# Kernel tuning notes

Measured on AMD Instinct MI355X. Metric: run time of the kernel, lower is better.

The kernel has to match this reference:

```python
import jax, jax.numpy as jnp
import numpy as np

D_MODEL = 256; D_STATE = 64; D_CONV = 4; EXPAND = 2; HEADDIM = 64; CHUNK = 64
D_INNER = EXPAND * D_MODEL          # 512
NHEADS = D_INNER // HEADDIM         # 8
D_IN_PROJ = 2 * D_INNER + 2 * D_STATE + NHEADS   # 1160
CONV_DIM = D_INNER + 2 * D_STATE    # 640
OBS_DIM = 3; T = 4096; BK = 32; K = 4


def setup_inputs() -> dict:
    key = jax.random.key(0)
    ks = jax.random.split(key, 8)
    f = jnp.float32
    return {
        "obs": jax.random.normal(ks[0], (T, BK, OBS_DIM), f),
        "W_in": jax.random.normal(ks[1], (D_MODEL, OBS_DIM), f) * 0.1,
        "b_in": jnp.zeros((D_MODEL,), f),
        "in_proj_w": jax.random.normal(ks[2], (D_IN_PROJ, D_MODEL), f) * 0.02,
        "conv_w": jax.random.normal(ks[3], (CONV_DIM, D_CONV), f) * 0.2,
        "conv_b": jnp.zeros((CONV_DIM,), f),
        "dt_bias": jax.random.normal(ks[4], (NHEADS,), f) * 0.1,
        "A_log": jnp.log(jnp.arange(1, NHEADS + 1, dtype=f)),
        "D_param": jnp.ones((NHEADS,), f),
        "norm_w": jnp.ones((D_INNER,), f),
        "out_proj_w": jax.random.normal(ks[5], (D_MODEL, D_INNER), f) * 0.02,
        "head": jnp.zeros((1,), f),
        "log_tau": jnp.zeros((1,), f),
        "k": K,
    }


def segsum(x):
    """Stable segment-sum: x (..., T) -> (..., T, T) lower-triangular cumulative sums."""
    L = x.shape[-1]
    x = jnp.broadcast_to(x[..., None], (*x.shape, L))
    x = jnp.where(jnp.tril(jnp.ones((L, L), bool), -1), x, 0.0)
    s = jnp.cumsum(x, axis=-2)
    return jnp.where(jnp.tril(jnp.ones((L, L), bool), 0), s, -jnp.inf)


def ssd(x, A, B, C, chunk):
    """Mamba2 SSD. x:(b,l,h,p) A:(b,l,h) B,C:(b,l,n). Returns y:(b,l,h,p), final state."""
    b, l, h, p = x.shape
    c = l // chunk
    x = x.reshape(b, c, chunk, h, p)
    A = A.reshape(b, c, chunk, h).transpose(0, 3, 1, 2)        # (b,h,c,l)
    B = B.reshape(b, c, chunk, -1)
    C = C.reshape(b, c, chunk, -1)
    A_cs = jnp.cumsum(A, axis=-1)                              # (b,h,c,l)
    Lmat = jnp.exp(segsum(A))                                  # (b,h,c,l,s)
    Y_diag = jnp.einsum('bcln,bcsn,bhcls,bcshp->bclhp', C, B, Lmat, x)
    decay_states = jnp.exp(A_cs[..., -1:] - A_cs)              # (b,h,c,l)
    states = jnp.einsum('bcln,bhcl,bclhp->bchpn', B, decay_states, x)
    states = jnp.concatenate([jnp.zeros_like(states[:, :1]), states], axis=1)
    decay_chunk = jnp.exp(segsum(jnp.pad(A_cs[..., -1], ((0, 0), (0, 0), (1, 0)))))
    new_states = jnp.einsum('bhzc,bchpn->bzhpn', decay_chunk, states)
    states, final = new_states[:, :-1], new_states[:, -1]
    Y_off = jnp.einsum('bcln,bchpn,bhcl->bclhp', C, states, jnp.exp(A_cs))
    return (Y_diag + Y_off).reshape(b, l, h, p), final


def reference(obs, W_in, b_in, in_proj_w, conv_w, conv_b, dt_bias, A_log, D_param,
              norm_w, out_proj_w, head, log_tau, k):
    Tt, Bk, _ = obs.shape
    x = obs @ W_in.T + b_in                        # (T,Bk,d_model)  input linear
    u = jnp.transpose(x, (1, 0, 2))                # (Bk,T,d_model)
    zxbcdt = u @ in_proj_w.T                       # (Bk,T,d_in_proj)
    z = zxbcdt[..., :D_INNER]
    xBC = zxbcdt[..., D_INNER:D_INNER + CONV_DIM]
    dt = jax.nn.softplus(zxbcdt[..., D_INNER + CONV_DIM:] + dt_bias)   # (B,T,h)
    # causal depthwise conv1d + silu (kernel D_CONV)
    xp = jnp.pad(xBC, ((0, 0), (D_CONV - 1, 0), (0, 0)))
    conv = conv_b
    for i in range(D_CONV):
        conv = conv + xp[:, i:i + Tt, :] * conv_w[:, i]
    xBC = jax.nn.silu(conv)
    xs = xBC[..., :D_INNER].reshape(Bk, Tt, NHEADS, HEADDIM)
    Bm = xBC[..., D_INNER:D_INNER + D_STATE]
    Cm = xBC[..., D_INNER + D_STATE:]
    A = -jnp.exp(A_log)                            # (h,)
    y, _final = ssd(xs * dt[..., None], A * dt, Bm, Cm, CHUNK)
    y = y + xs * D_param[None, None, :, None]
    y = y.reshape(Bk, Tt, D_INNER)
    # gated RMSNorm
    y = y * jax.nn.silu(z)
    y = y * jax.lax.rsqrt(jnp.mean(y * y, axis=-1, keepdims=True) + 1e-5) * norm_w
    y = y @ out_proj_w.T                           # (Bk,T,d_model)
    y = jnp.transpose(y, (1, 0, 2))                # (T,Bk,d_model)
    q = jnp.sum(y, axis=-1) * jax.nn.softplus(head)  # (T,Bk)
    q = q.reshape(Tt, -1, k)
    logits = q / jnp.exp(log_tau)
    return (q, logits)
```

## Files before the change

kernel.cpp:

```cpp
#include <hip/hip_runtime.h>

#define TLEN 4096
#define NBK  32

typedef __attribute__((ext_vector_type(8))) short short8;
typedef __attribute__((ext_vector_type(8))) unsigned short ushort8;
typedef __attribute__((ext_vector_type(4))) unsigned short ushort4v;
typedef __attribute__((ext_vector_type(4))) float f32x4;

#define OFF_WC 0
#define OFF_BC 3480
#define OFF_W3 4640
#define OFF_TB 12320
#define OFF_NW 14880
#define OFF_Y_BYTES 262144

__device__ __forceinline__ unsigned short f2bf(float f){
  unsigned int u = __float_as_uint(f);
  u = (u + 0x7FFFu + ((u >> 16) & 1u)) >> 16;
  return (unsigned short)u;
}
__device__ __forceinline__ float bf2f(unsigned short h){
  return __uint_as_float(((unsigned int)h) << 16);
}
__device__ __forceinline__ float softplusf_(float x){
  return (x > 15.f) ? x : log1pf(__expf(x));
}
__device__ __forceinline__ float siluf_(float x){
  return x * __fdividef(1.f, 1.f + __expf(-x));
}

__global__ void prep1_kernel(const float* __restrict__ ipw,
                             const float* __restrict__ W_in,
                             const float* __restrict__ b_in,
                             float* __restrict__ wsf){
  int r = blockIdx.x*256 + threadIdx.x;
  if (r >= 1160) return;
  const float* row = ipw + (size_t)r*256;
  float a0=0.f,a1=0.f,a2=0.f,ab=0.f;
  for (int m=0;m<256;m++){
    float w = row[m];
    a0 = fmaf(w, W_in[m*3+0], a0);
    a1 = fmaf(w, W_in[m*3+1], a1);
    a2 = fmaf(w, W_in[m*3+2], a2);
    ab = fmaf(w, b_in[m], ab);
  }
  wsf[OFF_WC + r*3+0]=a0; wsf[OFF_WC + r*3+1]=a1; wsf[OFF_WC + r*3+2]=a2;
  wsf[OFF_BC + r]=ab;
}

__global__ void prep2_kernel(const float* __restrict__ conv_w,
                             const float* __restrict__ norm_w,
                             const float* __restrict__ out_proj_w,
                             float* __restrict__ wsf){
  int r = blockIdx.x*256 + threadIdx.x;
  if (r < 640){
    float bc = wsf[OFF_BC + 512 + r];
    #pragma unroll
    for (int i=0;i<4;i++){
      float cw = conv_w[r*4+i];
      wsf[OFF_TB + r*4+i] = cw*bc;
      wsf[OFF_W3 + r*12 + i*3+0] = cw * wsf[OFF_WC + (512+r)*3+0];
      wsf[OFF_W3 + r*12 + i*3+1] = cw * wsf[OFF_WC + (512+r)*3+1];
      wsf[OFF_W3 + r*12 + i*3+2] = cw * wsf[OFF_WC + (512+r)*3+2];
    }
  }
  if (r < 512){
    float s=0.f;
    for (int m=0;m<256;m++) s += out_proj_w[(size_t)m*512 + r];
    wsf[OFF_NW + r] = norm_w[r]*s;
  }
}

#define SW(row_, col_) ((row_)*64 + ((col_) ^ (((row_)&7)<<3)))

__global__ __launch_bounds__(1024, 1) void ssd_kernel(
    const float* __restrict__ obs, const float* __restrict__ conv_b,
    const float* __restrict__ dt_bias, const float* __restrict__ A_log,
    const float* __restrict__ D_param, const float* __restrict__ wsf,
    unsigned short* __restrict__ Yg)
{
  __shared__ __align__(16) unsigned short obs_b[3*4096];
  __shared__ __align__(16) unsigned short W3T[192*40];
  __shared__ __align__(16) unsigned short OW[2][64*40];
  __shared__ float dt_l[4096];
  __shared__ float acs_l[4096];
  __shared__ float CBe[192];
  __shared__ float TBl[192*4];
  __shared__ __align__(16) unsigned short Bs[64*64], BDTl[64*64], Cs[64*64],
      CEl[64*64], XDT[64*64], XSl[64*64], Mm[64*64], Sb[64*64];

  const int tid  = threadIdx.x;
  const int b    = blockIdx.x >> 3;
  const int h    = blockIdx.x & 7;
  const int lane = tid & 63;
  const int wid  = tid >> 6;
  const int tm   = wid >> 2, tn = wid & 3;

  const int am    = tm*16 + (lane & 15);
  const int bn    = tn*16 + (lane & 15);
  const int rbase = tm*16 + ((lane>>4)&3)*4;

  for (int idx = tid; idx < 3*4096; idx += 1024){
    int j = idx >> 12, t = idx & 4095;
    obs_b[idx] = f2bf(obs[(size_t)t*(NBK*3) + b*3 + j]);
  }
  for (int idx = tid; idx < 192*28; idx += 1024){
    int row = idx/28; W3T[row*40 + 12 + (idx - row*28)] = 0;
  }
  for (int idx = tid; idx < 2*64*28; idx += 1024){
    int row = idx/28; (&OW[0][0])[row*40 + 12 + (idx - row*28)] = 0;
  }
  for (int idx = tid; idx < 192*12; idx += 1024){
    int lc = idx/12, ij = idx - lc*12;
    int ch = (lc<64) ? h*64+lc : 448+lc;
    W3T[lc*40 + ij] = f2bf(wsf[OFF_W3 + ch*12 + ij]);
  }
  for (int idx = tid; idx < 192; idx += 1024){
    int ch = (idx<64) ? h*64+idx : 448+idx;
    float s = conv_b[ch];
    #pragma unroll
    for (int i=0;i<4;i++){ float tb = wsf[OFF_TB + ch*4 + i]; TBl[idx*4+i] = tb; s += tb; }
    CBe[idx] = s;
  }
  const float Wd0 = wsf[OFF_WC+(1152+h)*3+0], Wd1 = wsf[OFF_WC+(1152+h)*3+1],
              Wd2 = wsf[OFF_WC+(1152+h)*3+2];
  const float bdt = wsf[OFF_BC + 1152 + h] + dt_bias[h];
  const float A_h = -__expf(A_log[h]);
  const float Dh  = D_param[h];
  for (int cc = wid; cc < 64; cc += 16){
    int t = cc*64 + lane;
    const float* ob = obs + (size_t)t*(NBK*3) + b*3;
    float draw = bdt + Wd0*ob[0] + Wd1*ob[1] + Wd2*ob[2];
    float dtv = softplusf_(draw);
    float a = A_h * dtv;
    #pragma unroll
    for (int o=1;o<64;o<<=1){
      float u = __shfl_up(a, o);
      if (lane >= o) a += u;
    }
    dt_l[t] = dtv; acs_l[t] = a;
  }
  __syncthreads();

  short8 afrag[3];
  #pragma unroll
  for (int e=0;e<3;e++){
    int idx = wid*3+e, ct = idx>>2;
    afrag[e] = *(const short8*)&W3T[(ct*16 + (lane&15))*40 + ((lane>>4)&3)*8];
  }
  if (tid < 768){
    int tt_ = tid/12, ij = tid - tt_*12;
    int i = ij/3, j = ij - i*3;
    int ts = tt_ - 3 + i;
    OW[0][tt_*40 + ij] = (ts >= 0) ? obs_b[j*4096 + ts] : (unsigned short)0;
  }
  __syncthreads();

  f32x4 sreg = {0.f,0.f,0.f,0.f};

  for (int c = 0; c < 64; ++c){
    const int t0 = c*64;
    const float At = acs_l[t0 + 63];

    {
      ushort4v sp;
      #pragma unroll
      for (int r=0;r<4;r++) sp[r] = f2bf(sreg[r]);
      *(ushort4v*)&Sb[SW(bn, rbase)] = sp;

      f32x4 g[3];
      #pragma unroll
      for (int e=0;e<3;e++){
        int idx = wid*3+e, tt = idx&3;
        const short8 bf = *(const short8*)&OW[c&1][(tt*16 + (lane&15))*40 + ((lane>>4)&3)*8];
        f32x4 z0 = {0.f,0.f,0.f,0.f};
        g[e] = __builtin_amdgcn_mfma_f32_16x16x32_bf16(afrag[e], bf, z0, 0, 0, 0);
      }
      #pragma unroll
      for (int e=0;e<3;e++){
        const int idx = wid*3+e, ct = idx>>2, tt = idx&3;
        const int t_  = tt*16 + (lane&15);
        const int chb = ct*16 + ((lane>>4)&3)*4;
        float dtt  = dt_l[t0 + t_];
        float acst = acs_l[t0 + t_];
        float dcy  = __expf(At - acst);
        float eAc  = __expf(acst);
        float v[4];
        #pragma unroll
        for (int r=0;r<4;r++){
          float pre = g[e][r] + CBe[chb+r];
          if (c==0 && tt==0){
            int tq = lane&15;
            if (tq < 3){
              #pragma unroll
              for (int i2=0;i2<3;i2++) if (i2 < 3-tq) pre -= TBl[(chb+r)*4+i2];
            }
          }
          v[r] = siluf_(pre);
        }
        if (ct < 4){
          int cb = chb;
          ushort4v xs_;
          #pragma unroll
          for (int r=0;r<4;r++) xs_[r] = f2bf(v[r]);
          *(ushort4v*)&XSl[SW(t_, cb)] = xs_;
          #pragma unroll
          for (int r=0;r<4;r++) XDT[SW(cb+r, t_)] = f2bf(v[r]*dtt);
        } else if (ct < 8){
          int nb = chb - 64;
          ushort4v b_;
          #pragma unroll
          for (int r=0;r<4;r++) b_[r] = f2bf(v[r]);
          *(ushort4v*)&Bs[SW(t_, nb)] = b_;
          #pragma unroll
          for (int r=0;r<4;r++) BDTl[SW(nb+r, t_)] = f2bf(v[r]*dcy);
        } else {
          int nb = chb - 128;
          ushort4v c_, ce_;
          #pragma unroll
          for (int r=0;r<4;r++){ c_[r] = f2bf(v[r]); ce_[r] = f2bf(v[r]*eAc); }
          *(ushort4v*)&Cs[SW(t_, nb)]  = c_;
          *(ushort4v*)&CEl[SW(t_, nb)] = ce_;
        }
      }
      if (c < 63 && tid < 768){
        int tt_ = tid/12, ij = tid - tt_*12;
        int i = ij/3, j = ij - i*3;
        int ts = (c+1)*64 + tt_ - 3 + i;
        OW[(c+1)&1][tt_*40 + ij] = obs_b[j*4096 + ts];
      }
    }
    __syncthreads();

    {
      f32x4 g2 = {0.f,0.f,0.f,0.f};
      #pragma unroll
      for (int k=0;k<2;k++){
        int kb = k*32 + ((lane>>4)&3)*8;
        const short8 av = *(const short8*)&Cs[SW(am, kb)];
        const short8 bv = *(const short8*)&Bs[SW(bn, kb)];
        g2 = __builtin_amdgcn_mfma_f32_16x16x32_bf16(av, bv, g2, 0, 0, 0);
      }
      float acS = acs_l[t0 + bn];
      #pragma unroll
      for (int r=0;r<4;r++){
        int lrow = rbase + r;
        float acl = acs_l[t0 + lrow];
        float mv = (lrow >= bn) ? g2[r]*__expf(acl - acS) : 0.f;
        Mm[SW(lrow, bn)] = f2bf(mv);
      }
    }
    __syncthreads();

    {
      f32x4 y = {0.f,0.f,0.f,0.f};
      #pragma unroll
      for (int k=0;k<2;k++){
        int kb = k*32 + ((lane>>4)&3)*8;
        const short8 av = *(const short8*)&Mm[SW(am, kb)];
        const short8 bv = *(const short8*)&XDT[SW(bn, kb)];
        y = __builtin_amdgcn_mfma_f32_16x16x32_bf16(av, bv, y, 0, 0, 0);
      }
      #pragma unroll
      for (int k=0;k<2;k++){
        int kb = k*32 + ((lane>>4)&3)*8;
        const short8 av = *(const short8*)&CEl[SW(am, kb)];
        const short8 bv = *(const short8*)&Sb[SW(bn, kb)];
        y = __builtin_amdgcn_mfma_f32_16x16x32_bf16(av, bv, y, 0, 0, 0);
      }
      float eAtot = __expf(At);
      #pragma unroll
      for (int r=0;r<4;r++) sreg[r] *= eAtot;
      #pragma unroll
      for (int k=0;k<2;k++){
        int kb = k*32 + ((lane>>4)&3)*8;
        const short8 av = *(const short8*)&BDTl[SW(am, kb)];
        const short8 bv = *(const short8*)&XDT[SW(bn, kb)];
        sreg = __builtin_amdgcn_mfma_f32_16x16x32_bf16(av, bv, sreg, 0, 0, 0);
      }
      #pragma unroll
      for (int r=0;r<4;r++){
        int lrow = rbase + r;
        float xsv = bf2f(XSl[SW(lrow, bn)]);
        Yg[((size_t)(b*4096 + t0 + lrow))*512 + h*64 + bn] = f2bf(y[r] + xsv*Dh);
      }
    }
    __syncthreads();
  }
}

__global__ __launch_bounds__(256) void final_kernel(
    const unsigned short* __restrict__ Yg, const float* __restrict__ obs,
    const float* __restrict__ wsf, const float* __restrict__ head,
    const float* __restrict__ log_tau, float* __restrict__ out)
{
  __shared__ float Wz[512*3];
  __shared__ float bz[512];
  __shared__ float nwl[512];
  int tid = threadIdx.x;
  for (int i=tid; i<512*3; i+=256) Wz[i] = wsf[OFF_WC + i];
  for (int i=tid; i<512; i+=256){ bz[i] = wsf[OFF_BC+i]; nwl[i] = wsf[OFF_NW+i]; }
  __syncthreads();
  int wid = tid>>6, lane = tid&63;
  float hsc  = softplusf_(head[0]);
  float itau = __expf(-log_tau[0]);
  int base = blockIdx.x*64 + wid*16;
  for (int rr=0; rr<16; ++rr){
    int row = base + rr;
    int bb = row >> 12, t = row & 4095;
    const float* ob = obs + (size_t)t*(NBK*3) + bb*3;
    float o0=ob[0], o1=ob[1], o2=ob[2];
    ushort8 yv = *(const ushort8*)&Yg[(size_t)row*512 + lane*8];
    float s2=0.f, sq=0.f;
    #pragma unroll
    for (int u=0;u<8;u++){
      int i = lane*8+u;
      float yf = bf2f(yv[u]);
      float z = bz[i] + Wz[i*3]*o0 + Wz[i*3+1]*o1 + Wz[i*3+2]*o2;
      float yg = yf * siluf_(z);
      s2 = fmaf(yg, yg, s2);
      sq = fmaf(yg, nwl[i], sq);
    }
    #pragma unroll
    for (int o=32;o;o>>=1){ s2 += __shfl_xor(s2,o); sq += __shfl_xor(sq,o); }
    if (lane==0){
      float rms = rsqrtf(s2*(1.f/512.f) + 1e-5f);
      float q = sq * rms * hsc;
      out[(size_t)t*32 + bb] = q;
      out[131072 + (size_t)t*32 + bb] = q * itau;
    }
  }
}

extern "C" void kernel_launch(void* const* d_in, const int* in_sizes, int n_in,
                              void* d_out, int out_size, void* d_ws, size_t ws_size,
                              hipStream_t stream) {
  (void)in_sizes; (void)n_in; (void)out_size; (void)ws_size;
  const float* obs        = (const float*)d_in[0];
  const float* W_in       = (const float*)d_in[1];
  const float* b_in       = (const float*)d_in[2];
  const float* in_proj_w  = (const float*)d_in[3];
  const float* conv_w     = (const float*)d_in[4];
  const float* conv_b     = (const float*)d_in[5];
  const float* dt_bias    = (const float*)d_in[6];
  const float* A_log      = (const float*)d_in[7];
  const float* D_param    = (const float*)d_in[8];
  const float* norm_w     = (const float*)d_in[9];
  const float* out_proj_w = (const float*)d_in[10];
  const float* head       = (const float*)d_in[11];
  const float* log_tau    = (const float*)d_in[12];
  float* wsf = (float*)d_ws;
  unsigned short* Yg = (unsigned short*)((char*)d_ws + OFF_Y_BYTES);
  float* out = (float*)d_out;

  prep1_kernel<<<5, 256, 0, stream>>>(in_proj_w, W_in, b_in, wsf);
  prep2_kernel<<<3, 256, 0, stream>>>(conv_w, norm_w, out_proj_w, wsf);
  ssd_kernel<<<256, 1024, 0, stream>>>(obs, conv_b, dt_bias, A_log, D_param, wsf, Yg);
  final_kernel<<<2048, 256, 0, stream>>>(Yg, obs, wsf, head, log_tau, out);
}
```

Baseline: 456.7 us.

## Double-buffer SSD chunk staging, fold D skip into diagonal, parallelize prep reductions

The SSD kernel now double-buffers the per-chunk B/C/X tiles. The conv projection for chunk c+1 (and the obs window for c+2) is computed while chunk c's matmuls run, so one barrier per chunk goes away. The D skip term is folded into the diagonal of the intra-chunk mask matrix, which removes the XS buffer. Decay exponentials are precomputed once, packed bf16 conversion instructions are used, and the obs staging buffer is dropped. prep1 switches to one wave per row with shuffle reductions, and final_kernel keeps its weights in registers and uses strided Yg loads. More shared memory is used, and folding D/dt into a bf16 matrix may cost precision.

```diff
diff --git a/kernel.cpp b/kernel.cpp
--- a/kernel.cpp
+++ b/kernel.cpp
@@ -1,12 +1,8 @@
 #include <hip/hip_runtime.h>
 
-#define TLEN 4096
-#define NBK  32
-
 typedef __attribute__((ext_vector_type(8))) short short8;
-typedef __attribute__((ext_vector_type(8))) unsigned short ushort8;
-typedef __attribute__((ext_vector_type(4))) unsigned short ushort4v;
 typedef __attribute__((ext_vector_type(4))) float f32x4;
+typedef __attribute__((ext_vector_type(2))) unsigned int uint2v;
 
 #define OFF_WC 0
 #define OFF_BC 3480
@@ -23,30 +19,46 @@
 __device__ __forceinline__ float bf2f(unsigned short h){
   return __uint_as_float(((unsigned int)h) << 16);
 }
+__device__ __forceinline__ unsigned int cvtpk(float lo, float hi){
+  unsigned int r;
+  asm("v_cvt_pk_bf16_f32 %0, %1, %2" : "=v"(r) : "v"(lo), "v"(hi));
+  return r;
+}
 __device__ __forceinline__ float softplusf_(float x){
   return (x > 15.f) ? x : log1pf(__expf(x));
 }
 __device__ __forceinline__ float siluf_(float x){
   return x * __fdividef(1.f, 1.f + __expf(-x));
 }
+
+#define SW(row_, col_) ((row_)*64 + ((col_) ^ (((row_)&7)<<3)))
 
 __global__ void prep1_kernel(const float* __restrict__ ipw,
                              const float* __restrict__ W_in,
                              const float* __restrict__ b_in,
                              float* __restrict__ wsf){
-  int r = blockIdx.x*256 + threadIdx.x;
-  if (r >= 1160) return;
-  const float* row = ipw + (size_t)r*256;
+  int gw = (blockIdx.x*256 + threadIdx.x) >> 6;
+  int lane = threadIdx.x & 63;
+  if (gw >= 1160) return;
+  const float* row = ipw + (size_t)gw*256;
   float a0=0.f,a1=0.f,a2=0.f,ab=0.f;
-  for (int m=0;m<256;m++){
+  #pragma unroll
+  for (int m = lane; m < 256; m += 64){
     float w = row[m];
     a0 = fmaf(w, W_in[m*3+0], a0);
     a1 = fmaf(w, W_in[m*3+1], a1);
     a2 = fmaf(w, W_in[m*3+2], a2);
     ab = fmaf(w, b_in[m], ab);
   }
-  wsf[OFF_WC + r*3+0]=a0; wsf[OFF_WC + r*3+1]=a1; wsf[OFF_WC + r*3+2]=a2;
-  wsf[OFF_BC + r]=ab;
+  #pragma unroll
+  for (int o=32;o;o>>=1){
+    a0 += __shfl_xor(a0,o); a1 += __shfl_xor(a1,o);
+    a2 += __shfl_xor(a2,o); ab += __shfl_xor(ab,o);
+  }
+  if (lane==0){
+    wsf[OFF_WC + gw*3+0]=a0; wsf[OFF_WC + gw*3+1]=a1; wsf[OFF_WC + gw*3+2]=a2;
+    wsf[OFF_BC + gw]=ab;
+  }
 }
 
 __global__ void prep2_kernel(const float* __restrict__ conv_w,
@@ -72,56 +84,60 @@
   }
 }
 
-#define SW(row_, col_) ((row_)*64 + ((col_) ^ (((row_)&7)<<3)))
-
-__global__ __launch_bounds__(1024, 1) void ssd_kernel(
+__global__ __launch_bounds__(1024, 4) void ssd_kernel(
     const float* __restrict__ obs, const float* __restrict__ conv_b,
     const float* __restrict__ dt_bias, const float* __restrict__ A_log,
     const float* __restrict__ D_param, const float* __restrict__ wsf,
     unsigned short* __restrict__ Yg)
 {
-  __shared__ __align__(16) unsigned short obs_b[3*4096];
-  __shared__ __align__(16) unsigned short W3T[192*40];
+  __shared__ __align__(16) float acs_l[4096];
+  __shared__ __align__(16) float dt_l[4096];
+  __shared__ __align__(16) unsigned short eAc_l[4096];
+  __shared__ __align__(16) unsigned short dcy_l[4096];
+  __shared__ __align__(16) unsigned short BsT[2*4096];
+  __shared__ __align__(16) unsigned short CsT[2*4096];
+  __shared__ __align__(16) unsigned short CET[2*4096];
+  __shared__ __align__(16) unsigned short XDTt[2*4096];
+  __shared__ __align__(16) unsigned short BDTt[2*4096];
+  __shared__ __align__(16) unsigned short MmSb[2*4096];
   __shared__ __align__(16) unsigned short OW[2][64*40];
-  __shared__ float dt_l[4096];
-  __shared__ float acs_l[4096];
   __shared__ float CBe[192];
-  __shared__ float TBl[192*4];
-  __shared__ __align__(16) unsigned short Bs[64*64], BDTl[64*64], Cs[64*64],
-      CEl[64*64], XDT[64*64], XSl[64*64], Mm[64*64], Sb[64*64];
 
   const int tid  = threadIdx.x;
   const int b    = blockIdx.x >> 3;
   const int h    = blockIdx.x & 7;
   const int lane = tid & 63;
   const int wid  = tid >> 6;
+  const int ln15 = lane & 15;
+  const int quad = (lane >> 4) & 3;
+  const int quad4 = quad*4, quad8 = quad*8;
   const int tm   = wid >> 2, tn = wid & 3;
-
-  const int am    = tm*16 + (lane & 15);
-  const int bn    = tn*16 + (lane & 15);
-  const int rbase = tm*16 + ((lane>>4)&3)*4;
-
-  for (int idx = tid; idx < 3*4096; idx += 1024){
-    int j = idx >> 12, t = idx & 4095;
-    obs_b[idx] = f2bf(obs[(size_t)t*(NBK*3) + b*3 + j]);
-  }
-  for (int idx = tid; idx < 192*28; idx += 1024){
-    int row = idx/28; W3T[row*40 + 12 + (idx - row*28)] = 0;
-  }
-  for (int idx = tid; idx < 2*64*28; idx += 1024){
-    int row = idx/28; (&OW[0][0])[row*40 + 12 + (idx - row*28)] = 0;
-  }
-  for (int idx = tid; idx < 192*12; idx += 1024){
-    int lc = idx/12, ij = idx - lc*12;
-    int ch = (lc<64) ? h*64+lc : 448+lc;
-    W3T[lc*40 + ij] = f2bf(wsf[OFF_W3 + ch*12 + ij]);
-  }
-  for (int idx = tid; idx < 192; idx += 1024){
-    int ch = (idx<64) ? h*64+idx : 448+idx;
+  const int am    = tm*16 + ln15;
+  const int bn    = tn*16 + ln15;
+  const int rbase = tm*16 + quad4;
+
+  unsigned short* const Mm  = MmSb;
+  unsigned short* const Sb  = MmSb + 4096;
+  unsigned short* const W3T = MmSb;
+
+  for (int i = tid; i < 192*40; i += 1024){
+    int lc = i/40, k = i - lc*40;
+    unsigned short v = 0;
+    if (k < 12){
+      int ch = (lc<64) ? h*64+lc : 448+lc;
+      v = f2bf(wsf[OFF_W3 + ch*12 + k]);
+    }
+    W3T[i] = v;
+  }
+  for (int i = tid; i < 2*64*28; i += 1024){
+    int r = i/28; (&OW[0][0])[r*40 + 12 + (i - r*28)] = 0;
+  }
+  if (tid < 192){
+    int ch = (tid<64) ? h*64+tid : 448+tid;
     float s = conv_b[ch];
     #pragma unroll
-    for (int i=0;i<4;i++){ float tb = wsf[OFF_TB + ch*4 + i]; TBl[idx*4+i] = tb; s += tb; }
-    CBe[idx] = s;
+    for (int i=0;i<4;i++) s += wsf[OFF_TB + ch*4 + i];
+    CBe[tid] = s;
   }
   const float Wd0 = wsf[OFF_WC+(1152+h)*3+0], Wd1 = wsf[OFF_WC+(1152+h)*3+1],
               Wd2 = wsf[OFF_WC+(1152+h)*3+2];
@@ -130,7 +146,7 @@
   const float Dh  = D_param[h];
   for (int cc = wid; cc < 64; cc += 16){
     int t = cc*64 + lane;
-    const float* ob = obs + (size_t)t*(NBK*3) + b*3;
+    const float* ob = obs + (size_t)t*96 + b*3;
     float draw = bdt + Wd0*ob[0] + Wd1*ob[1] + Wd2*ob[2];
     float dtv = softplusf_(draw);
     float a = A_h * dtv;
@@ -139,151 +155,182 @@
       float u = __shfl_up(a, o);
       if (lane >= o) a += u;
     }
-    dt_l[t] = dtv; acs_l[t] = a;
+    float At = __shfl(a, 63);
+    dt_l[t]  = dtv;
+    acs_l[t] = a;
+    eAc_l[t] = f2bf(__expf(a));
+    dcy_l[t] = f2bf(__expf(At - a));
   }
   __syncthreads();
 
-  short8 afrag[3];
+  short8 afrag1[2], afrag2[2];
+  float  cbe1[2][4], cbe2[2];
   #pragma unroll
-  for (int e=0;e<3;e++){
-    int idx = wid*3+e, ct = idx>>2;
-    afrag[e] = *(const short8*)&W3T[(ct*16 + (lane&15))*40 + ((lane>>4)&3)*8];
-  }
-  if (tid < 768){
-    int tt_ = tid/12, ij = tid - tt_*12;
-    int i = ij/3, j = ij - i*3;
-    int ts = tt_ - 3 + i;
-    OW[0][tt_*40 + ij] = (ts >= 0) ? obs_b[j*4096 + ts] : (unsigned short)0;
-  }
+  for (int e=0;e<2;e++){
+    const int idx = wid*2+e;
+    const int ct1 = 4 + (idx & 7);
+    afrag1[e] = *(const short8*)&W3T[(ct1*16 + ln15)*40 + quad8];
+    #pragma unroll
+    for (int r=0;r<4;r++) cbe1[e][r] = CBe[ct1*16 + quad4 + r];
+    const int ct2 = idx & 7;
+    afrag2[e] = *(const short8*)&W3T[(ct2*16 + ln15)*40 + quad8];
+    cbe2[e] = CBe[ct2*16 + ln15];
+  }
+
+  auto PREFOW = [&](int cn){
+    if (tid < 768){
+      int tt_ = tid/12, ij = tid - tt_*12;
+      int i = ij/3, j = ij - i*3;
+      int ts = cn*64 + tt_ - 3 + i;
+      OW[cn&1][tt_*40 + ij] = (ts >= 0) ? f2bf(obs[(size_t)ts*96 + b*3 + j])
+                                        : (unsigned short)0;
+    }
+  };
+  PREFOW(0);
+  PREFOW(1);
   __syncthreads();
 
-  f32x4 sreg = {0.f,0.f,0.f,0.f};
-
-  for (int c = 0; c < 64; ++c){
-    const int t0 = c*64;
-    const float At = acs_l[t0 + 63];
-
-    {
-      ushort4v sp;
-      #pragma unroll
-      for (int r=0;r<4;r++) sp[r] = f2bf(sreg[r]);
-      *(ushort4v*)&Sb[SW(bn, rbase)] = sp;
-
-      f32x4 g[3];
-      #pragma unroll
-      for (int e=0;e<3;e++){
-        int idx = wid*3+e, tt = idx&3;
-        const short8 bf = *(const short8*)&OW[c&1][(tt*16 + (lane&15))*40 + ((lane>>4)&3)*8];
+  auto STAGE = [&](int cn, int pn){
+    unsigned short* Bp  = BsT  + pn*4096;
+    unsigned short* Cp  = CsT  + pn*4096;
+    unsigned short* CEp = CET  + pn*4096;
+    unsigned short* Xp  = XDTt + pn*4096;
+    unsigned short* BDp = BDTt + pn*4096;
+    const int tW0 = cn*64;
+    #pragma unroll
+    for (int e=0;e<2;e++){
+      const int idx = wid*2+e;
+      const int tt  = idx >> 3;
+      const short8 owf = *(const short8*)&OW[cn&1][(tt*16 + ln15)*40 + quad8];
+      {
+        const int ct1 = 4 + (idx & 7);
+        const int chb = ct1*16 + quad4;
+        const int t_  = tt*16 + ln15;
         f32x4 z0 = {0.f,0.f,0.f,0.f};
-        g[e] = __builtin_amdgcn_mfma_f32_16x16x32_bf16(afrag[e], bf, z0, 0, 0, 0);
-      }
-      #pragma unroll
-      for (int e=0;e<3;e++){
-        const int idx = wid*3+e, ct = idx>>2, tt = idx&3;
-        const int t_  = tt*16 + (lane&15);
-        const int chb = ct*16 + ((lane>>4)&3)*4;
-        float dtt  = dt_l[t0 + t_];
-        float acst = acs_l[t0 + t_];
-        float dcy  = __expf(At - acst);
-        float eAc  = __expf(acst);
+        f32x4 g = __builtin_amdgcn_mfma_f32_16x16x32_bf16(afrag1[e], owf, z0, 0,0,0);
         float v[4];
         #pragma unroll
         for (int r=0;r<4;r++){
-          float pre = g[e][r] + CBe[chb+r];
-          if (c==0 && tt==0){
-            int tq = lane&15;
-            if (tq < 3){
-              #pragma unroll
-              for (int i2=0;i2<3;i2++) if (i2 < 3-tq) pre -= TBl[(chb+r)*4+i2];
-            }
+          float pre = g[r] + cbe1[e][r];
+          if (cn==0 && tt==0 && ln15 < 3){
+            int chg = 448 + chb + r;
+            #pragma unroll
+            for (int i2=0;i2<3;i2++) if (i2 < 3-ln15) pre -= wsf[OFF_TB + chg*4 + i2];
           }
           v[r] = siluf_(pre);
         }
-        if (ct < 4){
-          int cb = chb;
-          ushort4v xs_;
-          #pragma unroll
-          for (int r=0;r<4;r++) xs_[r] = f2bf(v[r]);
-          *(ushort4v*)&XSl[SW(t_, cb)] = xs_;
-          #pragma unroll
-          for (int r=0;r<4;r++) XDT[SW(cb+r, t_)] = f2bf(v[r]*dtt);
-        } else if (ct < 8){
+        if (ct1 < 8){
           int nb = chb - 64;
-          ushort4v b_;
-          #pragma unroll
-          for (int r=0;r<4;r++) b_[r] = f2bf(v[r]);
-          *(ushort4v*)&Bs[SW(t_, nb)] = b_;
-          #pragma unroll
-          for (int r=0;r<4;r++) BDTl[SW(nb+r, t_)] = f2bf(v[r]*dcy);
+          *(uint2v*)&Bp[SW(t_, nb)] = (uint2v){cvtpk(v[0],v[1]), cvtpk(v[2],v[3])};
         } else {
           int nb = chb - 128;
-          ushort4v c_, ce_;
-          #pragma unroll
-          for (int r=0;r<4;r++){ c_[r] = f2bf(v[r]); ce_[r] = f2bf(v[r]*eAc); }
-          *(ushort4v*)&Cs[SW(t_, nb)]  = c_;
-          *(ushort4v*)&CEl[SW(t_, nb)] = ce_;
+          *(uint2v*)&Cp[SW(t_, nb)] = (uint2v){cvtpk(v[0],v[1]), cvtpk(v[2],v[3])};
+          float ea = bf2f(eAc_l[tW0 + t_]);
+          *(uint2v*)&CEp[SW(t_, nb)] =
+            (uint2v){cvtpk(v[0]*ea, v[1]*ea), cvtpk(v[2]*ea, v[3]*ea)};
         }
       }
-      if (c < 63 && tid < 768){
-        int tt_ = tid/12, ij = tid - tt_*12;
-        int i = ij/3, j = ij - i*3;
-        int ts = (c+1)*64 + tt_ - 3 + i;
-        OW[(c+1)&1][tt_*40 + ij] = obs_b[j*4096 + ts];
-      }
-    }
-    __syncthreads();
-
+      {
+        const int ct2 = idx & 7;
+        const int ch2 = ct2*16 + ln15;
+        const int tb2 = tt*16 + quad4;
+        f32x4 z0 = {0.f,0.f,0.f,0.f};
+        f32x4 g = __builtin_amdgcn_mfma_f32_16x16x32_bf16(owf, afrag2[e], z0, 0,0,0);
+        float v[4];
+        #pragma unroll
+        for (int r=0;r<4;r++){
+          float pre = g[r] + cbe2[e];
+          if (cn==0 && tt==0 && quad==0 && r<3){
+            int chg = (ch2<64) ? h*64+ch2 : 448+ch2;
+            #pragma unroll
+            for (int i2=0;i2<3;i2++) if (i2 < 3-r) pre -= wsf[OFF_TB + chg*4 + i2];
+          }
+          v[r] = siluf_(pre);
+        }
+        if (ct2 < 4){
+          float m0 = v[0]*dt_l[tW0+tb2+0], m1 = v[1]*dt_l[tW0+tb2+1];
+          float m2 = v[2]*dt_l[tW0+tb2+2], m3 = v[3]*dt_l[tW0+tb2+3];
+          *(uint2v*)&Xp[SW(ch2, tb2)] = (uint2v){cvtpk(m0,m1), cvtpk(m2,m3)};
+        } else {
+          int nb = ch2 - 64;
+          float m0 = v[0]*bf2f(dcy_l[tW0+tb2+0]), m1 = v[1]*bf2f(dcy_l[tW0+tb2+1]);
+          float m2 = v[2]*bf2f(dcy_l[tW0+tb2+2]), m3 = v[3]*bf2f(dcy_l[tW0+tb2+3]);
+          *(uint2v*)&BDp[SW(nb, tb2)] = (uint2v){cvtpk(m0,m1), cvtpk(m2,m3)};
+        }
+      }
+    }
+  };
+
+  STAGE(0, 0);
+  __syncthreads();
+
+  f32x4 sreg = {0.f,0.f,0.f,0.f};
+
+  for (int c = 0; c < 64; ++c){
+    const int t0 = c*64;
+    const int p  = c & 1;
+    const unsigned short* Bp  = BsT  + p*4096;
+    const unsigned short* Cp  = CsT  + p*4096;
+    const unsigned short* CEp = CET  + p*4096;
+    const unsigned short* Xp  = XDTt + p*4096;
+    const unsigned short* BDp = BDTt + p*4096;
+
+    *(uint2v*)&Sb[SW(bn, rbase)] = (uint2v){cvtpk(sreg[0],sreg[1]), cvtpk(sreg[2],sreg[3])};
+    if (c < 63) STAGE(c+1, (c+1)&1);
+    if (c < 62) PREFOW(c+2);
     {
       f32x4 g2 = {0.f,0.f,0.f,0.f};
       #pragma unroll
       for (int k=0;k<2;k++){
-        int kb = k*32 + ((lane>>4)&3)*8;
-        const short8 av = *(const short8*)&Cs[SW(am, kb)];
-        const short8 bv = *(const short8*)&Bs[SW(bn, kb)];
+        int kb = k*32 + quad8;
+        const short8 av = *(const short8*)&Bp[SW(am, kb)];
+        const short8 bv = *(const short8*)&Cp[SW(bn, kb)];
         g2 = __builtin_amdgcn_mfma_f32_16x16x32_bf16(av, bv, g2, 0, 0, 0);
       }
-      float acS = acs_l[t0 + bn];
+      float acB  = acs_l[t0 + bn];
+      float diag = __fdividef(Dh, dt_l[t0 + bn]);
+      float mv[4];
       #pragma unroll
       for (int r=0;r<4;r++){
-        int lrow = rbase + r;
-        float acl = acs_l[t0 + lrow];
-        float mv = (lrow >= bn) ? g2[r]*__expf(acl - acS) : 0.f;
-        Mm[SW(lrow, bn)] = f2bf(mv);
-      }
+        int srow = rbase + r;
+        float m_ = (bn >= srow) ? g2[r]*__expf(acB - acs_l[t0 + srow]) : 0.f;
+        if (bn == srow) m_ += diag;
+        mv[r] = m_;
+      }
+      *(uint2v*)&Mm[SW(bn, rbase)] = (uint2v){cvtpk(mv[0],mv[1]), cvtpk(mv[2],mv[3])};
     }
     __syncthreads();
 
     {
+      short8 xf[2];
+      #pragma unroll
+      for (int k=0;k<2;k++) xf[k] = *(const short8*)&Xp[SW(bn, k*32 + quad8)];
       f32x4 y = {0.f,0.f,0.f,0.f};
       #pragma unroll
       for (int k=0;k<2;k++){
-        int kb = k*32 + ((lane>>4)&3)*8;
+        int kb = k*32 + quad8;
         const short8 av = *(const short8*)&Mm[SW(am, kb)];
-        const short8 bv = *(const short8*)&XDT[SW(bn, kb)];
-        y = __builtin_amdgcn_mfma_f32_16x16x32_bf16(av, bv, y, 0, 0, 0);
+        y = __builtin_amdgcn_mfma_f32_16x16x32_bf16(av, xf[k], y, 0, 0, 0);
       }
       #pragma unroll
       for (int k=0;k<2;k++){
-        int kb = k*32 + ((lane>>4)&3)*8;
-        const short8 av = *(const short8*)&CEl[SW(am, kb)];
+        int kb = k*32 + quad8;
+        const short8 av = *(const short8*)&CEp[SW(am, kb)];
         const short8 bv = *(const short8*)&Sb[SW(bn, kb)];
         y = __builtin_amdgcn_mfma_f32_16x16x32_bf16(av, bv, y, 0, 0, 0);
       }
-      float eAtot = __expf(At);
+      float eAtot = __expf(acs_l[t0 + 63]);
       #pragma unroll
       for (int r=0;r<4;r++) sreg[r] *= eAtot;
       #pragma unroll
       for (int k=0;k<2;k++){
-        int kb = k*32 + ((lane>>4)&3)*8;
-        const short8 av = *(const short8*)&BDTl[SW(am, kb)];
-        const short8 bv = *(const short8*)&XDT[SW(bn, kb)];
-        sreg = __builtin_amdgcn_mfma_f32_16x16x32_bf16(av, bv, sreg, 0, 0, 0);
+        int kb = k*32 + quad8;
+        const short8 av = *(const short8*)&BDp[SW(am, kb)];
+        sreg = __builtin_amdgcn_mfma_f32_16x16x32_bf16(av, xf[k], sreg, 0, 0, 0);
       }
       #pragma unroll
       for (int r=0;r<4;r++){
-        int lrow = rbase + r;
-        float xsv = bf2f(XSl[SW(lrow, bn)]);
-        Yg[((size_t)(b*4096 + t0 + lrow))*512 + h*64 + bn] = f2bf(y[r] + xsv*Dh);
+        Yg[((size_t)(b*4096 + t0 + rbase + r))*512 + h*64 + bn] = f2bf(y[r]);
       }
     }
     __syncthreads();
@@ -295,32 +342,34 @@
     const float* __restrict__ wsf, const float* __restrict__ head,
     const float* __restrict__ log_tau, float* __restrict__ out)
 {
-  __shared__ float Wz[512*3];
-  __shared__ float bz[512];
-  __shared__ float nwl[512];
   int tid = threadIdx.x;
-  for (int i=tid; i<512*3; i+=256) Wz[i] = wsf[OFF_WC + i];
-  for (int i=tid; i<512; i+=256){ bz[i] = wsf[OFF_BC+i]; nwl[i] = wsf[OFF_NW+i]; }
-  __syncthreads();
-  int wid = tid>>6, lane = tid&63;
+  int wv = tid >> 6, lane = tid & 63;
+  float zw0[8], zw1[8], zw2[8], zb[8], znw[8];
+  #pragma unroll
+  for (int u=0;u<8;u++){
+    int ch = u*64 + lane;
+    zw0[u] = wsf[OFF_WC + ch*3+0];
+    zw1[u] = wsf[OFF_WC + ch*3+1];
+    zw2[u] = wsf[OFF_WC + ch*3+2];
+    zb[u]  = wsf[OFF_BC + ch];
+    znw[u] = wsf[OFF_NW + ch];
+  }
   float hsc  = softplusf_(head[0]);
   float itau = __expf(-log_tau[0]);
-  int base = blockIdx.x*64 + wid*16;
+  int base = blockIdx.x*64 + wv*16;
   for (int rr=0; rr<16; ++rr){
     int row = base + rr;
     int bb = row >> 12, t = row & 4095;
-    const float* ob = obs + (size_t)t*(NBK*3) + bb*3;
+    const float* ob = obs + (size_t)t*96 + bb*3;
     float o0=ob[0], o1=ob[1], o2=ob[2];
-    ushort8 yv = *(const ushort8*)&Yg[(size_t)row*512 + lane*8];
     float s2=0.f, sq=0.f;
     #pragma unroll
     for (int u=0;u<8;u++){
-      int i = lane*8+u;
-      float yf = bf2f(yv[u]);
-      float z = bz[i] + Wz[i*3]*o0 + Wz[i*3+1]*o1 + Wz[i*3+2]*o2;
+      float yf = bf2f(Yg[(size_t)row*512 + u*64 + lane]);
+      float z  = zb[u] + zw0[u]*o0 + zw1[u]*o1 + zw2[u]*o2;
       float yg = yf * siluf_(z);
       s2 = fmaf(yg, yg, s2);
-      sq = fmaf(yg, nwl[i], sq);
+      sq = fmaf(yg, znw[u], sq);
     }
     #pragma unroll
     for (int o=32;o;o>>=1){ s2 += __shfl_xor(s2,o); sq += __shfl_xor(sq,o); }
@@ -354,7 +403,7 @@
   unsigned short* Yg = (unsigned short*)((char*)d_ws + OFF_Y_BYTES);
   float* out = (float*)d_out;
 
-  prep1_kernel<<<5, 256, 0, stream>>>(in_proj_w, W_in, b_in, wsf);
+  prep1_kernel<<<290, 256, 0, stream>>>(in_proj_w, W_in, b_in, wsf);
   prep2_kernel<<<3, 256, 0, stream>>>(conv_w, norm_w, out_proj_w, wsf);
   ssd_kernel<<<256, 1024, 0, stream>>>(obs, conv_b, dt_bias, A_log, D_param, wsf, Yg);
   final_kernel<<<2048, 256, 0, stream>>>(Yg, obs, wsf, head, log_tau, out);
```

Result: faster. 391.1 us (-14.4%).
